# Optimization experiments

Measured on AMD Instinct MI355X. Metric: run time of the kernel, lower is better.

## Reference

```python
import jax, jax.numpy as jnp
import numpy as np

T = 8  # hardcoded temporal window in the original forward

def setup_inputs() -> dict:
    key = jax.random.key(0)
    ks = jax.random.split(key, 9)
    C = 256
    Ch = C // 2
    feat = jax.random.normal(ks[0], (32, C, 28, 28), dtype=jnp.float32)
    s = 0.02
    return {
        "feat": feat,
        "theta_w": jax.random.normal(ks[1], (Ch, C), dtype=jnp.float32) * s,
        "theta_b": jax.random.normal(ks[2], (Ch,), dtype=jnp.float32) * s,
        "phi_w": jax.random.normal(ks[3], (Ch, C), dtype=jnp.float32) * s,
        "phi_b": jax.random.normal(ks[4], (Ch,), dtype=jnp.float32) * s,
        "g_w": jax.random.normal(ks[5], (Ch, C), dtype=jnp.float32) * s,
        "g_b": jax.random.normal(ks[6], (Ch,), dtype=jnp.float32) * s,
        "embed_w": jax.random.normal(ks[7], (C, Ch), dtype=jnp.float32) * s,
        "embed_b": jax.random.normal(ks[8], (C,), dtype=jnp.float32) * s,
    }

def reference(feat, theta_w, theta_b, phi_w, phi_b, g_w, g_b, embed_w, embed_b):
    BT, C, H, W = feat.shape
    b = BT // T
    # (B*T, C, H, W) -> (b, T, C, H, W) -> (b, C, T, H, W) -> flatten space-time
    x = feat.reshape(b, T, C, H, W).transpose(0, 2, 1, 3, 4)
    N = T * H * W
    xf = x.reshape(b, C, N)
    # 1x1x1 Conv3d == per-position linear projection
    theta = jnp.einsum('oc,bcn->bon', theta_w, xf) + theta_b[:, None]   # (b, C/2, N)
    phi   = jnp.einsum('oc,bcn->bon', phi_w,   xf) + phi_b[:, None]     # (b, C/2, N)
    g     = jnp.einsum('oc,bcn->bon', g_w,     xf) + g_b[:, None]       # (b, C/2, N)
    # attention[b,i,j] = sum_c phi[b,c,i] * theta[b,c,j]; softmax over dim=1 (i axis)
    att = jax.nn.softmax(jnp.einsum('bci,bcj->bij', phi, theta), axis=1)  # (b, N, N)
    y = jnp.einsum('bcn,bnm->bcm', g, att)                               # (b, C/2, N)
    out = jnp.einsum('oc,bcn->bon', embed_w, y) + embed_b[:, None]       # (b, C, N)
    new_feat = out.reshape(b, C, T, H, W).transpose(0, 2, 1, 3, 4).reshape(BT, C, H, W)
    return feat + new_feat
```

## Files before the change

### kernel.cpp

```cpp
#include <hip/hip_runtime.h>
#include <hip/hip_bf16.h>

#define NTOK 6272
#define HW   784
#define NB   4
#define NROW (NB * NTOK)

typedef __bf16 bf16x8 __attribute__((ext_vector_type(8)));
typedef float  f32x4  __attribute__((ext_vector_type(4)));
typedef float  f32x16 __attribute__((ext_vector_type(16)));
typedef long   longx2 __attribute__((ext_vector_type(2)));

__device__ __forceinline__ f32x4 mfma16(bf16x8 a, bf16x8 b, f32x4 c) {
    return __builtin_amdgcn_mfma_f32_16x16x32_bf16(a, b, c, 0, 0, 0);
}
__device__ __forceinline__ f32x16 mfma32(bf16x8 a, bf16x8 b, f32x16 c) {
    return __builtin_amdgcn_mfma_f32_32x32x16_bf16(a, b, c, 0, 0, 0);
}
__device__ __forceinline__ f32x16 mfma32f8(long a, long b, f32x16 c) {
    return __builtin_amdgcn_mfma_f32_32x32x16_fp8_fp8(a, b, c, 0, 0, 0);
}

#define GLDS(gsrc, ldst) \
    __builtin_amdgcn_global_load_lds((const __attribute__((address_space(1))) void*)(gsrc), \
        (__attribute__((address_space(3))) void*)(ldst), 16, 0, 0)

#if __has_builtin(__builtin_amdgcn_exp2f)
#define EXP2(x) __builtin_amdgcn_exp2f(x)
#else
#define EXP2(x) __expf((x) * 0.6931471805599453f)
#endif

template<int N> struct ic { static constexpr int value = N; };

__device__ __forceinline__ unsigned pkbf(float a, float b) {
    __bf16 l = (__bf16)a, h = (__bf16)b;
    unsigned short ul, uh;
    __builtin_memcpy(&ul, &l, 2);
    __builtin_memcpy(&uh, &h, 2);
    return (unsigned)ul | ((unsigned)uh << 16);
}

__device__ __forceinline__ unsigned pk4f8(float a, float b, float c, float d) {
    unsigned u = (unsigned)__builtin_amdgcn_cvt_pk_fp8_f32(a, b, 0, false);
    u = (unsigned)__builtin_amdgcn_cvt_pk_fp8_f32(c, d, (int)u, true);
    return u;
}

__device__ __forceinline__ void pl32swap(unsigned &a, unsigned &b) {
    asm volatile("v_permlane32_swap_b32 %0, %1" : "+v"(a), "+v"(b));
}
__device__ __forceinline__ float xhalf_sum(float x) {
    unsigned a = __float_as_uint(x), b = a;
    pl32swap(a, b);
    return __uint_as_float(a) + __uint_as_float(b);
}

__global__ void prep_kernel(const float* __restrict__ tw, const float* __restrict__ pw,
                            const float* __restrict__ gw, const float* __restrict__ ew,
                            __hip_bfloat16* __restrict__ Wf, __hip_bfloat16* __restrict__ EWb) {
    int gid = blockIdx.x * 256 + threadIdx.x;
    if (gid < 98304) {
        int j = gid & 7, lane = (gid >> 3) & 63, kk = (gid >> 9) & 15, mt = gid >> 13;
        int mat = mt >> 2;
        int o = (mt & 3) * 32 + (lane & 31);
        int c = kk * 16 + (lane >> 5) * 8 + j;
        const float* src = (mat == 0) ? tw : (mat == 1) ? pw : gw;
        Wf[gid] = __float2bfloat16(src[o * 256 + c]);
    } else {
        int t = gid - 98304;
        if (t < 32768) EWb[t] = __float2bfloat16(ew[t]);
    }
}

__global__ void __launch_bounds__(256, 3)
proj_kernel(const float* __restrict__ feat, const __hip_bfloat16* __restrict__ Wf,
            const float* __restrict__ tb, const float* __restrict__ pb,
            const float* __restrict__ gb,
            unsigned char* __restrict__ Q8, unsigned char* __restrict__ K8,
            __hip_bfloat16* __restrict__ VT) {
    __shared__ __hip_bfloat16 Xt[32 * 256];
    int blk = blockIdx.x;
    int bi = blk / 196, c32 = blk % 196;
    int n0 = c32 * 32;
    int tid = threadIdx.x;

    {
        int n_l = tid & 31;
        int c0g = tid >> 5;
        int n_b = n0 + n_l;
        int t = n_b / HW, hw = n_b % HW;
        const float* fb = feat + ((size_t)(bi * 8 + t) * 256) * HW + hw;
#pragma unroll
        for (int ii = 0; ii < 4; ii++) {
            int chunk = c0g + ii * 8;
            int cb = chunk * 8;
            union { unsigned u[4]; bf16x8 v; } pu;
#pragma unroll
            for (int p = 0; p < 4; p++) {
                float f0 = fb[(size_t)(cb + 2 * p) * HW];
                float f1 = fb[(size_t)(cb + 2 * p + 1) * HW];
                pu.u[p] = pkbf(f0, f1);
            }
            int chs = chunk ^ n_l;
            *reinterpret_cast<bf16x8*>((char*)Xt + n_l * 512 + chs * 16) = pu.v;
        }
    }
    __syncthreads();

    int w = tid >> 6, lane = tid & 63, q32 = lane & 31, hi = lane >> 5;
    f32x16 acc[3];
#pragma unroll
    for (int m = 0; m < 3; m++) acc[m] = {};

    const char* Xc = (const char*)Xt;
#pragma unroll
    for (int kk = 0; kk < 16; kk++) {
        int chs = (kk * 2 + hi) ^ q32;
        bf16x8 bfr = *reinterpret_cast<const bf16x8*>(Xc + q32 * 512 + chs * 16);
#pragma unroll
        for (int m = 0; m < 3; m++) {
            int mt = m * 4 + w;
            bf16x8 af = *reinterpret_cast<const bf16x8*>(Wf + ((size_t)(mt * 16 + kk) * 64 + lane) * 8);
            acc[m] = mfma32(af, bfr, acc[m]);
        }
    }

    size_t bq8 = (size_t)bi * NTOK * 128;
    size_t bq  = (size_t)bi * NTOK * 128;
    int n_b = n0 + q32;
#pragma unroll
    for (int m = 0; m < 2; m++) {
        unsigned char* dst = (m == 0 ? Q8 : K8) + bq8 + (size_t)n_b * 128;
        const float* bias = (m == 0) ? tb : pb;
#pragma unroll
        for (int q2 = 0; q2 < 4; q2++) {
            int ob = w * 32 + q2 * 8 + hi * 4;
            float v0 = acc[m][q2 * 4 + 0] + bias[ob + 0];
            float v1 = acc[m][q2 * 4 + 1] + bias[ob + 1];
            float v2 = acc[m][q2 * 4 + 2] + bias[ob + 2];
            float v3 = acc[m][q2 * 4 + 3] + bias[ob + 3];
            if (m == 0) { v0 *= 1.44269504f; v1 *= 1.44269504f; v2 *= 1.44269504f; v3 *= 1.44269504f; }
            int pos = ((ob >> 3) & 1) * 64 + (ob >> 4) * 8 + (ob & 7);
            *reinterpret_cast<unsigned*>(dst + pos) = pk4f8(v0, v1, v2, v3);
        }
    }
#pragma unroll
    for (int r = 0; r < 16; r++) {
        int o = w * 32 + (r & 3) + 8 * (r >> 2) + 4 * hi;
        VT[bq + (size_t)o * NTOK + n_b] = __float2bfloat16(acc[2][r] + gb[o]);
    }
}

template<int S>
__global__ void __launch_bounds__(256, 2)
attn_kernel(const unsigned char* __restrict__ Qg, const unsigned char* __restrict__ Kg,
            const __hip_bfloat16* __restrict__ Vg, __hip_bfloat16* __restrict__ Out,
            float* __restrict__ lpart) {
    __shared__ alignas(16) unsigned char Kt8[2][64 * 128];
    __shared__ alignas(16) __hip_bfloat16 Vt[2][64 * 128];

    int bid = blockIdx.x;
    int s   = bid % S;
    int qc  = (bid / S) % 49;
    int bi  = bid / (S * 49);
    int qbase = qc * 128;
    int kt0 = (98 * s) / S, kt1 = (98 * (s + 1)) / S;

    int tid  = threadIdx.x;
    int w    = tid >> 6;
    int lane = tid & 63;
    int q32  = lane & 31;
    int hi   = lane >> 5;

    const unsigned char* Qb = Qg + (size_t)bi * NTOK * 128;
    const unsigned char* Kb = Kg + (size_t)bi * NTOK * 128;
    const __hip_bfloat16* Vb = Vg + (size_t)bi * NTOK * 128;

    long qf8[8];
    {
        const unsigned char* qrow = Qb + (size_t)(qbase + w * 32 + q32) * 128 + hi * 64;
#pragma unroll
        for (int kkp = 0; kkp < 4; kkp++) {
            longx2 qq = *reinterpret_cast<const longx2*>(qrow + kkp * 16);
            qf8[2 * kkp] = qq[0];
            qf8[2 * kkp + 1] = qq[1];
        }
    }

    int k0 = q32 * 256 + (((hi * 4) ^ (q32 & 15)) * 16);
    int r2 = q32 >> 1;
    int v0b = r2 * 256 + ((((q32 & 1) * 8 + hi) ^ r2) * 16);

    float l_run = 0.f;
    f32x16 oacc[4];
#pragma unroll
    for (int ct = 0; ct < 4; ct++) oacc[ct] = {};

    auto stage_K = [&](int c, int kb) {
#pragma unroll
        for (int i = 0; i < 2; i++) {
            int seg = w * 2 + i;
            int chunk_lds = seg * 64 + lane;
            int r = chunk_lds >> 4;
            int c16 = (chunk_lds & 15) ^ (r & 15);
            int kh = c16 >> 3;
            int ck = c16 & 7;
            const unsigned char* src = Kb + (size_t)(kb + kh * 32 + r) * 128 + ck * 16;
            GLDS(src, &Kt8[c][seg * 1024]);
        }
    };
    auto stage_V = [&](int c, int kb) {
#pragma unroll
        for (int i = 0; i < 4; i++) {
            int seg = w * 4 + i;
            int row = seg * 4 + (lane >> 4);
            int chunk = (lane & 15) ^ (row & 15);
            int ch = row * 2 + (chunk >> 3);
            int k8 = chunk & 7;
            const __hip_bfloat16* src = Vb + (size_t)ch * NTOK + kb + k8 * 8;
            GLDS(src, &Vt[c][seg * 512]);
        }
    };

    const char* KB8 = (const char*)&Kt8[0][0];
    const char* VB0 = (const char*)&Vt[0][0];

    auto body = [&](auto CURC, int nt) {
        constexpr int CUR = decltype(CURC)::value;
        if (nt + 1 < kt1) {
            stage_K(CUR ^ 1, (nt + 1) * 64);
            stage_V(CUR ^ 1, (nt + 1) * 64);
        }

        f32x16 st0 = {}, st1 = {};
        __builtin_amdgcn_s_setprio(1);
#pragma unroll
        for (int kkp = 0; kkp < 4; kkp++) {
            longx2 a0 = *reinterpret_cast<const longx2*>(KB8 + CUR * 8192 + (k0 ^ (kkp * 16)));
            longx2 a1 = *reinterpret_cast<const longx2*>(KB8 + CUR * 8192 + (k0 ^ (kkp * 16 + 128)));
            st0 = mfma32f8(a0[0], qf8[2 * kkp], st0);
            st1 = mfma32f8(a1[0], qf8[2 * kkp], st1);
            st0 = mfma32f8(a0[1], qf8[2 * kkp + 1], st0);
            st1 = mfma32f8(a1[1], qf8[2 * kkp + 1], st1);
        }
        __builtin_amdgcn_s_setprio(0);

        float ps = 0.f;
#pragma unroll
        for (int j = 0; j < 16; j++) { st0[j] = EXP2(st0[j]); ps += st0[j]; }
#pragma unroll
        for (int j = 0; j < 16; j++) { st1[j] = EXP2(st1[j]); ps += st1[j]; }
        l_run += ps;

        bf16x8 pf[4];
#pragma unroll
        for (int hf = 0; hf < 2; hf++) {
#pragma unroll
            for (int p = 0; p < 2; p++) {
                float e0, e1, e2, e3, e4, e5, e6, e7;
                if (hf == 0) {
                    e0 = st0[p*8+0]; e1 = st0[p*8+1]; e2 = st0[p*8+2]; e3 = st0[p*8+3];
                    e4 = st0[p*8+4]; e5 = st0[p*8+5]; e6 = st0[p*8+6]; e7 = st0[p*8+7];
                } else {
                    e0 = st1[p*8+0]; e1 = st1[p*8+1]; e2 = st1[p*8+2]; e3 = st1[p*8+3];
                    e4 = st1[p*8+4]; e5 = st1[p*8+5]; e6 = st1[p*8+6]; e7 = st1[p*8+7];
                }
                unsigned A0 = pkbf(e0, e1);
                unsigned A1 = pkbf(e2, e3);
                unsigned A2 = pkbf(e4, e5);
                unsigned A3 = pkbf(e6, e7);
                pl32swap(A0, A2);
                pl32swap(A1, A3);
                union { unsigned u[4]; bf16x8 v; } pu;
                pu.u[0] = A0; pu.u[1] = A1; pu.u[2] = A2; pu.u[3] = A3;
                pf[hf * 2 + p] = pu.v;
            }
        }

        __builtin_amdgcn_s_setprio(1);
#pragma unroll
        for (int ct = 0; ct < 4; ct++) {
#pragma unroll
            for (int ss = 0; ss < 4; ss++) {
                bf16x8 av = *reinterpret_cast<const bf16x8*>(
                    VB0 + CUR * 16384 + ct * 4096 + (v0b ^ (ss * 32)));
                oacc[ct] = mfma32(av, pf[ss], oacc[ct]);
            }
        }
        __builtin_amdgcn_s_setprio(0);

        __syncthreads();
    };

    stage_K(0, kt0 * 64);
    stage_V(0, kt0 * 64);
    __syncthreads();

    int nt = kt0;
    for (; nt + 1 < kt1; nt += 2) {
        body(ic<0>{}, nt);
        body(ic<1>{}, nt + 1);
    }
    if (nt < kt1) body(ic<0>{}, nt);

    float l_tot = xhalf_sum(l_run);
    float invl = 1.f / l_tot;
    size_t orow = (size_t)bi * NTOK + qbase + w * 32 + q32;
    size_t obase = (S == 1) ? orow * 128 : ((size_t)s * NROW + orow) * 128;
#pragma unroll
    for (int ct = 0; ct < 4; ct++)
#pragma unroll
        for (int u = 0; u < 4; u++) {
            int c = ct * 32 + u * 8 + 4 * hi;
            union { unsigned uu[2]; uint2 d; } pk2;
            pk2.uu[0] = pkbf(oacc[ct][4 * u + 0] * invl, oacc[ct][4 * u + 1] * invl);
            pk2.uu[1] = pkbf(oacc[ct][4 * u + 2] * invl, oacc[ct][4 * u + 3] * invl);
            *reinterpret_cast<uint2*>(&Out[obase + c]) = pk2.d;
        }
    if (S > 1 && hi == 0)
        lpart[(size_t)s * NROW + orow] = l_tot;
}

template<int S>
__global__ void __launch_bounds__(256)
embed_kernel(const __hip_bfloat16* __restrict__ EWb, const __hip_bfloat16* __restrict__ Opart,
             const float* __restrict__ lpart, const float* __restrict__ eb,
             const float* __restrict__ feat, float* __restrict__ out) {
    __shared__ __hip_bfloat16 Yt[32 * 128];
    int bi = blockIdx.x / 196;
    int c32 = blockIdx.x % 196;
    int nbase = c32 * 32;
    int tid = threadIdx.x;

    {
        int row = tid >> 3, q = tid & 7;
        size_t grow = (size_t)bi * NTOK + nbase + row;
        float wgt[S];
        if (S > 1) {
            float den = 0.f;
#pragma unroll
            for (int s = 0; s < S; s++) { wgt[s] = lpart[(size_t)s * NROW + grow]; den += wgt[s]; }
            float inv = 1.f / den;
#pragma unroll
            for (int s = 0; s < S; s++) wgt[s] *= inv;
        }
#pragma unroll
        for (int k = 0; k < 2; k++) {
            int kc = q + 8 * k;
            union { unsigned u[4]; bf16x8 v; } pu;
            if (S == 1) {
                pu.v = *reinterpret_cast<const bf16x8*>(&Opart[grow * 128 + kc * 8]);
            } else {
                float o8[8];
#pragma unroll
                for (int j = 0; j < 8; j++) o8[j] = 0.f;
#pragma unroll
                for (int s = 0; s < S; s++) {
                    bf16x8 v = *reinterpret_cast<const bf16x8*>(
                        &Opart[((size_t)s * NROW + grow) * 128 + kc * 8]);
#pragma unroll
                    for (int j = 0; j < 8; j++) o8[j] = fmaf(wgt[s], (float)v[j], o8[j]);
                }
#pragma unroll
                for (int p = 0; p < 4; p++) pu.u[p] = pkbf(o8[2 * p], o8[2 * p + 1]);
            }
            int chs = kc ^ (row & 15);
            *reinterpret_cast<bf16x8*>((char*)Yt + row * 256 + chs * 16) = pu.v;
        }
    }
    __syncthreads();

    int w = tid >> 6, lane = tid & 63, ln = lane & 15, g = lane >> 4;
    f32x4 acc[4][2];
#pragma unroll
    for (int rt = 0; rt < 4; rt++)
#pragma unroll
        for (int ct = 0; ct < 2; ct++) acc[rt][ct] = (f32x4){0.f, 0.f, 0.f, 0.f};

    const char* Yc = (const char*)Yt;
#pragma unroll
    for (int ks = 0; ks < 4; ks++) {
        bf16x8 A[4], Bv[2];
#pragma unroll
        for (int rt = 0; rt < 4; rt++)
            A[rt] = *reinterpret_cast<const bf16x8*>(
                &EWb[(size_t)(w * 64 + rt * 16 + ln) * 128 + ks * 32 + g * 8]);
#pragma unroll
        for (int ct = 0; ct < 2; ct++) {
            int row = ct * 16 + ln;
            int chs = (ks * 4 + g) ^ (row & 15);
            Bv[ct] = *reinterpret_cast<const bf16x8*>(Yc + row * 256 + chs * 16);
        }
#pragma unroll
        for (int rt = 0; rt < 4; rt++)
#pragma unroll
            for (int ct = 0; ct < 2; ct++)
                acc[rt][ct] = mfma16(A[rt], Bv[ct], acc[rt][ct]);
    }

#pragma unroll
    for (int rt = 0; rt < 4; rt++)
#pragma unroll
        for (int ct = 0; ct < 2; ct++)
#pragma unroll
            for (int r = 0; r < 4; r++) {
                int c = w * 64 + rt * 16 + g * 4 + r;
                int n = nbase + ct * 16 + ln;
                int t = n / HW, sp = n % HW;
                size_t idx = ((size_t)(bi * 8 + t) * 256 + c) * HW + sp;
                out[idx] = feat[idx] + acc[rt][ct][r] + eb[c];
            }
}

extern "C" void kernel_launch(void* const* d_in, const int* in_sizes, int n_in,
                              void* d_out, int out_size, void* d_ws, size_t ws_size,
                              hipStream_t stream) {
    const float* feat = (const float*)d_in[0];
    const float* tw   = (const float*)d_in[1];
    const float* tb   = (const float*)d_in[2];
    const float* pw   = (const float*)d_in[3];
    const float* pb   = (const float*)d_in[4];
    const float* gw   = (const float*)d_in[5];
    const float* gb   = (const float*)d_in[6];
    const float* ew   = (const float*)d_in[7];
    const float* eb   = (const float*)d_in[8];
    float* out = (float*)d_out;

    const size_t NE = (size_t)NB * NTOK * 128;
    unsigned char* Q8 = (unsigned char*)d_ws;
    unsigned char* K8 = Q8 + NE;
    __hip_bfloat16* VT  = (__hip_bfloat16*)(K8 + NE);
    __hip_bfloat16* Wf  = VT + NE;
    __hip_bfloat16* EWb = Wf + 98304;
    __hip_bfloat16* Opart = EWb + 32768;

    const size_t base_bytes = (size_t)((char*)(Opart) - (char*)d_ws);
    const size_t per_split = (size_t)NROW * 128 * 2 + (size_t)NROW * 4;
    int S = 1;
    if (ws_size >= base_bytes + 8 * per_split) S = 8;
    else if (ws_size >= base_bytes + 4 * per_split) S = 4;
    else if (ws_size >= base_bytes + 2 * per_split) S = 2;

    float* lpart = (float*)(Opart + (size_t)S * NROW * 128);

    prep_kernel<<<512, 256, 0, stream>>>(tw, pw, gw, ew, Wf, EWb);
    proj_kernel<<<NB * 196, 256, 0, stream>>>(feat, Wf, tb, pb, gb, Q8, K8, VT);

    if (S == 8) {
        attn_kernel<8><<<NB * 49 * 8, 256, 0, stream>>>(Q8, K8, VT, Opart, lpart);
        embed_kernel<8><<<NB * 196, 256, 0, stream>>>(EWb, Opart, lpart, eb, feat, out);
    } else if (S == 4) {
        attn_kernel<4><<<NB * 49 * 4, 256, 0, stream>>>(Q8, K8, VT, Opart, lpart);
        embed_kernel<4><<<NB * 196, 256, 0, stream>>>(EWb, Opart, lpart, eb, feat, out);
    } else if (S == 2) {
        attn_kernel<2><<<NB * 49 * 2, 256, 0, stream>>>(Q8, K8, VT, Opart, lpart);
        embed_kernel<2><<<NB * 196, 256, 0, stream>>>(EWb, Opart, lpart, eb, feat, out);
    } else {
        attn_kernel<1><<<NB * 49, 256, 0, stream>>>(Q8, K8, VT, Opart, nullptr);
        embed_kernel<1><<<NB * 196, 256, 0, stream>>>(EWb, Opart, lpart, eb, feat, out);
    }
}
```

Before: 147.7 us.

## Quantize V and attention probabilities to FP8 for the PV matmul

The projection kernel now writes V as FP8 in a blocked transposed layout instead of bf16. The attention kernel stages V in half the LDS bytes and computes P·V with fp8 32x32x16 MFMAs. P is exponentiated with a fixed offset (exp2(s-6)) to keep it in FP8 range. This halves V memory traffic and LDS footprint and uses the faster fp8 MFMA path, at the cost of lower precision in P and V and reliance on the fixed offset to avoid overflow or underflow.

After: 137.1 us. 7.2% less time.

```diff
diff --git a/kernel.cpp b/kernel.cpp
--- a/kernel.cpp
+++ b/kernel.cpp
@@ -30,6 +30,8 @@
 #else
 #define EXP2(x) __expf((x) * 0.6931471805599453f)
 #endif
+
+#define P_OFF 6.0f
 
 template<int N> struct ic { static constexpr int value = N; };
 
@@ -78,7 +80,7 @@
             const float* __restrict__ tb, const float* __restrict__ pb,
             const float* __restrict__ gb,
             unsigned char* __restrict__ Q8, unsigned char* __restrict__ K8,
-            __hip_bfloat16* __restrict__ VT) {
+            unsigned char* __restrict__ V8) {
     __shared__ __hip_bfloat16 Xt[32 * 256];
     int blk = blockIdx.x;
     int bi = blk / 196, c32 = blk % 196;
@@ -127,7 +129,6 @@
     }
 
     size_t bq8 = (size_t)bi * NTOK * 128;
-    size_t bq  = (size_t)bi * NTOK * 128;
     int n_b = n0 + q32;
 #pragma unroll
     for (int m = 0; m < 2; m++) {
@@ -145,20 +146,32 @@
             *reinterpret_cast<unsigned*>(dst + pos) = pk4f8(v0, v1, v2, v3);
         }
     }
-#pragma unroll
-    for (int r = 0; r < 16; r++) {
-        int o = w * 32 + (r & 3) + 8 * (r >> 2) + 4 * hi;
-        VT[bq + (size_t)o * NTOK + n_b] = __float2bfloat16(acc[2][r] + gb[o]);
+    {
+        int blk64 = n_b >> 6, k = n_b & 63;
+        int h = (k >> 3) & 1;
+        int pos = h * 32 + ((k >> 5) & 1) * 16 + ((k >> 4) & 1) * 8 + (k & 7);
+        unsigned char* vb = V8 + bq8 + (size_t)blk64 * 64 + pos;
+#pragma unroll
+        for (int q2 = 0; q2 < 4; q2++) {
+            int o0 = w * 32 + q2 * 8 + hi * 4;
+            unsigned pk = pk4f8(acc[2][q2 * 4 + 0] + gb[o0 + 0],
+                                acc[2][q2 * 4 + 1] + gb[o0 + 1],
+                                acc[2][q2 * 4 + 2] + gb[o0 + 2],
+                                acc[2][q2 * 4 + 3] + gb[o0 + 3]);
+#pragma unroll
+            for (int i = 0; i < 4; i++)
+                vb[(size_t)(o0 + i) * NTOK] = (unsigned char)(pk >> (8 * i));
+        }
     }
 }
 
 template<int S>
 __global__ void __launch_bounds__(256, 2)
 attn_kernel(const unsigned char* __restrict__ Qg, const unsigned char* __restrict__ Kg,
-            const __hip_bfloat16* __restrict__ Vg, __hip_bfloat16* __restrict__ Out,
+            const unsigned char* __restrict__ Vg, __hip_bfloat16* __restrict__ Out,
             float* __restrict__ lpart) {
     __shared__ alignas(16) unsigned char Kt8[2][64 * 128];
-    __shared__ alignas(16) __hip_bfloat16 Vt[2][64 * 128];
+    __shared__ alignas(16) unsigned char Vt8[2][64 * 128];
 
     int bid = blockIdx.x;
     int s   = bid % S;
@@ -175,7 +188,7 @@
 
     const unsigned char* Qb = Qg + (size_t)bi * NTOK * 128;
     const unsigned char* Kb = Kg + (size_t)bi * NTOK * 128;
-    const __hip_bfloat16* Vb = Vg + (size_t)bi * NTOK * 128;
+    const unsigned char* Vb = Vg + (size_t)bi * NTOK * 128;
 
     long qf8[8];
     {
@@ -189,8 +202,7 @@
     }
 
     int k0 = q32 * 256 + (((hi * 4) ^ (q32 & 15)) * 16);
-    int r2 = q32 >> 1;
-    int v0b = r2 * 256 + ((((q32 & 1) * 8 + hi) ^ r2) * 16);
+    int vbase = q32 * 256 + (((hi * 2) ^ (q32 & 15)) * 16);
 
     float l_run = 0.f;
     f32x16 oacc[4];
@@ -201,9 +213,9 @@
 #pragma unroll
         for (int i = 0; i < 2; i++) {
             int seg = w * 2 + i;
-            int chunk_lds = seg * 64 + lane;
-            int r = chunk_lds >> 4;
-            int c16 = (chunk_lds & 15) ^ (r & 15);
+            int q = seg * 64 + lane;
+            int r = q >> 4;
+            int c16 = (q & 15) ^ (r & 15);
             int kh = c16 >> 3;
             int ck = c16 & 7;
             const unsigned char* src = Kb + (size_t)(kb + kh * 32 + r) * 128 + ck * 16;
@@ -212,19 +224,21 @@
     };
     auto stage_V = [&](int c, int kb) {
 #pragma unroll
-        for (int i = 0; i < 4; i++) {
-            int seg = w * 4 + i;
-            int row = seg * 4 + (lane >> 4);
-            int chunk = (lane & 15) ^ (row & 15);
-            int ch = row * 2 + (chunk >> 3);
-            int k8 = chunk & 7;
-            const __hip_bfloat16* src = Vb + (size_t)ch * NTOK + kb + k8 * 8;
-            GLDS(src, &Vt[c][seg * 512]);
+        for (int i = 0; i < 2; i++) {
+            int seg = w * 2 + i;
+            int q = seg * 64 + lane;
+            int r = q >> 4;
+            int c16 = (q & 15) ^ (r & 15);
+            int ct = c16 >> 2;
+            int hh = (c16 >> 1) & 1;
+            int ssp = c16 & 1;
+            const unsigned char* src = Vb + (size_t)(ct * 32 + r) * NTOK + kb + hh * 32 + ssp * 16;
+            GLDS(src, &Vt8[c][seg * 1024]);
         }
     };
 
     const char* KB8 = (const char*)&Kt8[0][0];
-    const char* VB0 = (const char*)&Vt[0][0];
+    const char* VB8 = (const char*)&Vt8[0][0];
 
     auto body = [&](auto CURC, int nt) {
         constexpr int CUR = decltype(CURC)::value;
@@ -248,12 +262,12 @@
 
         float ps = 0.f;
 #pragma unroll
-        for (int j = 0; j < 16; j++) { st0[j] = EXP2(st0[j]); ps += st0[j]; }
-#pragma unroll
-        for (int j = 0; j < 16; j++) { st1[j] = EXP2(st1[j]); ps += st1[j]; }
+        for (int j = 0; j < 16; j++) { st0[j] = EXP2(st0[j] - P_OFF); ps += st0[j]; }
+#pragma unroll
+        for (int j = 0; j < 16; j++) { st1[j] = EXP2(st1[j] - P_OFF); ps += st1[j]; }
         l_run += ps;
 
-        bf16x8 pf[4];
+        long pf8[4];
 #pragma unroll
         for (int hf = 0; hf < 2; hf++) {
 #pragma unroll
@@ -266,15 +280,12 @@
                     e0 = st1[p*8+0]; e1 = st1[p*8+1]; e2 = st1[p*8+2]; e3 = st1[p*8+3];
                     e4 = st1[p*8+4]; e5 = st1[p*8+5]; e6 = st1[p*8+6]; e7 = st1[p*8+7];
                 }
-                unsigned A0 = pkbf(e0, e1);
-                unsigned A1 = pkbf(e2, e3);
-                unsigned A2 = pkbf(e4, e5);
-                unsigned A3 = pkbf(e6, e7);
-                pl32swap(A0, A2);
-                pl32swap(A1, A3);
-                union { unsigned u[4]; bf16x8 v; } pu;
-                pu.u[0] = A0; pu.u[1] = A1; pu.u[2] = A2; pu.u[3] = A3;
-                pf[hf * 2 + p] = pu.v;
+                unsigned P0 = pk4f8(e0, e1, e2, e3);
+                unsigned P1 = pk4f8(e4, e5, e6, e7);
+                pl32swap(P0, P1);
+                union { unsigned u[2]; long l; } pu;
+                pu.u[0] = P0; pu.u[1] = P1;
+                pf8[hf * 2 + p] = pu.l;
             }
         }
 
@@ -282,10 +293,11 @@
 #pragma unroll
         for (int ct = 0; ct < 4; ct++) {
 #pragma unroll
-            for (int ss = 0; ss < 4; ss++) {
-                bf16x8 av = *reinterpret_cast<const bf16x8*>(
-                    VB0 + CUR * 16384 + ct * 4096 + (v0b ^ (ss * 32)));
-                oacc[ct] = mfma32(av, pf[ss], oacc[ct]);
+            for (int ssp = 0; ssp < 2; ssp++) {
+                longx2 av = *reinterpret_cast<const longx2*>(
+                    VB8 + CUR * 8192 + (vbase ^ (ct << 6) ^ (ssp << 4)));
+                oacc[ct] = mfma32f8(av[0], pf8[2 * ssp], oacc[ct]);
+                oacc[ct] = mfma32f8(av[1], pf8[2 * ssp + 1], oacc[ct]);
             }
         }
         __builtin_amdgcn_s_setprio(0);
@@ -430,8 +442,8 @@
     const size_t NE = (size_t)NB * NTOK * 128;
     unsigned char* Q8 = (unsigned char*)d_ws;
     unsigned char* K8 = Q8 + NE;
-    __hip_bfloat16* VT  = (__hip_bfloat16*)(K8 + NE);
-    __hip_bfloat16* Wf  = VT + NE;
+    unsigned char* V8 = K8 + NE;
+    __hip_bfloat16* Wf  = (__hip_bfloat16*)(V8 + NE);
     __hip_bfloat16* EWb = Wf + 98304;
     __hip_bfloat16* Opart = EWb + 32768;
 
@@ -445,19 +457,19 @@
     float* lpart = (float*)(Opart + (size_t)S * NROW * 128);
 
     prep_kernel<<<512, 256, 0, stream>>>(tw, pw, gw, ew, Wf, EWb);
-    proj_kernel<<<NB * 196, 256, 0, stream>>>(feat, Wf, tb, pb, gb, Q8, K8, VT);
+    proj_kernel<<<NB * 196, 256, 0, stream>>>(feat, Wf, tb, pb, gb, Q8, K8, V8);
 
     if (S == 8) {
-        attn_kernel<8><<<NB * 49 * 8, 256, 0, stream>>>(Q8, K8, VT, Opart, lpart);
+        attn_kernel<8><<<NB * 49 * 8, 256, 0, stream>>>(Q8, K8, V8, Opart, lpart);
         embed_kernel<8><<<NB * 196, 256, 0, stream>>>(EWb, Opart, lpart, eb, feat, out);
     } else if (S == 4) {
-        attn_kernel<4><<<NB * 49 * 4, 256, 0, stream>>>(Q8, K8, VT, Opart, lpart);
+        attn_kernel<4><<<NB * 49 * 4, 256, 0, stream>>>(Q8, K8, V8, Opart, lpart);
         embed_kernel<4><<<NB * 196, 256, 0, stream>>>(EWb, Opart, lpart, eb, feat, out);
     } else if (S == 2) {
-        attn_kernel<2><<<NB * 49 * 2, 256, 0, stream>>>(Q8, K8, VT, Opart, lpart);
+        attn_kernel<2><<<NB * 49 * 2, 256, 0, stream>>>(Q8, K8, V8, Opart, lpart);
         embed_kernel<2><<<NB * 196, 256, 0, stream>>>(EWb, Opart, lpart, eb, feat, out);
     } else {
-        attn_kernel<1><<<NB * 49, 256, 0, stream>>>(Q8, K8, VT, Opart, nullptr);
+        attn_kernel<1><<<NB * 49, 256, 0, stream>>>(Q8, K8, V8, Opart, nullptr);
         embed_kernel<1><<<NB * 196, 256, 0, stream>>>(EWb, Opart, lpart, eb, feat, out);
     }
 }
```
